# Kernel tuning notes

Hardware: AMD Instinct MI355X
Metric: run time of the kernel (lower is better)

## Reference

```python
import jax, jax.numpy as jnp
import numpy as np
from jax import lax

B, T, CIN, FN, H, W = 8, 8, 64, 64, 32, 32
GROUPS = 4 * FN // 32  # 8


def group_norm(x, g, b, groups, eps=1e-5):
    Bn, C, Hh, Ww = x.shape
    xr = x.reshape(Bn, groups, C // groups, Hh, Ww)
    mu = xr.mean(axis=(2, 3, 4), keepdims=True)
    var = xr.var(axis=(2, 3, 4), keepdims=True)
    xn = ((xr - mu) * lax.rsqrt(var + eps)).reshape(Bn, C, Hh, Ww)
    return xn * g[None, :, None, None] + b[None, :, None, None]


def conv1x1(x, w, b):
    # x: [B,C,H,W], w: [O,C]
    return jnp.einsum('bchw,oc->bohw', x, w) + b[None, :, None, None]


def setup_inputs() -> dict:
    key = jax.random.key(0)
    ks = jax.random.split(key, 8)
    s = 0.05
    return {
        'inputs': jax.random.normal(ks[0], (B, T, CIN, H, W), jnp.float32),
        'conv_w': jax.random.normal(ks[1], (4 * FN, CIN + FN, 3, 3), jnp.float32) * s,
        'conv_b': jnp.zeros((4 * FN,), jnp.float32),
        'gn_g': jnp.ones((4 * FN,), jnp.float32),
        'gn_b': jnp.zeros((4 * FN,), jnp.float32),
        'h_w': jax.random.normal(ks[2], (3 * FN, FN), jnp.float32) * s,
        'h_b': jnp.zeros((3 * FN,), jnp.float32),
        'm_w': jax.random.normal(ks[3], (2 * FN, FN), jnp.float32) * s,
        'm_b': jnp.zeros((2 * FN,), jnp.float32),
        'z1_w': jax.random.normal(ks[4], (FN, 2 * FN), jnp.float32) * s,
        'z1_b': jnp.zeros((FN,), jnp.float32),
        'z2_w': jax.random.normal(ks[5], (3 * FN, 2 * FN), jnp.float32) * s,
        'z2_b': jnp.zeros((3 * FN,), jnp.float32),
    }


def _sam(oh, im, h_w, h_b, m_w, m_b, z1_w, z1_b, z2_w, z2_b):
    Bn, C, Hh, Ww = oh.shape
    HW = Hh * Ww
    h_qkv = conv1x1(oh, h_w, h_b)  # [B,3C,H,W]
    m_kv = conv1x1(im, m_w, m_b)   # [B,2C,H,W]
    Qh, Kh, Vh = jnp.split(h_qkv, 3, axis=1)
    Km, Vm = jnp.split(m_kv, 2, axis=1)
    Q = Qh.reshape(Bn, C, HW).transpose(0, 2, 1)  # [B,HW,C]
    Kh = Kh.reshape(Bn, C, HW)
    Vh = Vh.reshape(Bn, C, HW)
    Km = Km.reshape(Bn, C, HW)
    Vm = Vm.reshape(Bn, C, HW)
    Ah = jax.nn.softmax(jnp.einsum('bnc,bcm->bnm', Q, Kh), axis=-1)  # [B,HW,HW]
    Am = jax.nn.softmax(jnp.einsum('bnc,bcm->bnm', Q, Km), axis=-1)
    Zh = jnp.einsum('bcn,bnm->bcm', Vh, Ah)  # [B,C,HW]
    Zm = jnp.einsum('bcn,bnm->bcm', Vm, Am)
    Zcat = jnp.concatenate([Zh, Zm], axis=1).reshape(Bn, 2 * C, Hh, Ww)
    Z = conv1x1(Zcat, z1_w, z1_b)  # [B,C,H,W]
    gates = conv1x1(jnp.concatenate([Z, oh], axis=1), z2_w, z2_b)  # [B,3C,H,W]
    o, g, i = jnp.split(gates, 3, axis=1)
    i = jax.nn.sigmoid(i)
    om = jnp.tanh(g) * i + (1.0 - i) * im
    oh2 = jax.nn.sigmoid(o) * om
    return oh2, om


def reference(inputs, conv_w, conv_b, gn_g, gn_b, h_w, h_b, m_w, m_b, z1_w, z1_b, z2_w, z2_b):
    Bn = inputs.shape[0]
    Hh, Ww = inputs.shape[-2], inputs.shape[-1]
    ih0 = jnp.zeros((Bn, FN, Hh, Ww), inputs.dtype)
    ic0 = jnp.zeros_like(ih0)
    im0 = jnp.zeros_like(ih0)

    def step(carry, x):
        ih, ic, im = carry
        comb = jnp.concatenate([x, ih], axis=1)
        gates = lax.conv_general_dilated(
            comb, conv_w, window_strides=(1, 1), padding='SAME',
            dimension_numbers=('NCHW', 'OIHW', 'NCHW')) + conv_b[None, :, None, None]
        gates = group_norm(gates, gn_g, gn_b, GROUPS)
        ingate, forgetgate, cellgate, outgate = jnp.split(gates, 4, axis=1)
        oc = ic * jax.nn.sigmoid(forgetgate) + jax.nn.sigmoid(ingate) * jnp.tanh(cellgate)
        oh = jax.nn.sigmoid(outgate) * jnp.tanh(oc)
        oh, om = _sam(oh, im, h_w, h_b, m_w, m_b, z1_w, z1_b, z2_w, z2_b)
        return (oh, oc, om), oh

    xs = jnp.moveaxis(inputs, 1, 0)  # [T,B,C,H,W]
    (ohT, ocT, imT), ys = lax.scan(step, (ih0, ic0, im0), xs)
    out = jnp.moveaxis(ys, 0, 1)  # [B,T,FN,H,W]
    return out, (ohT, ocT, imT)
```

## Files before the change

kernel.cpp:

```cpp
#include <hip/hip_runtime.h>
#include <math.h>


#define DEV __device__ __forceinline__

DEV float sigm(float x) { return 1.0f / (1.0f + __expf(-x)); }

DEV unsigned short f2bf(float f) {
  union { float f; unsigned u; } v; v.f = f;
  unsigned r = v.u + 0x7FFF + ((v.u >> 16) & 1);
  return (unsigned short)(r >> 16);
}

DEV unsigned pk2(float a, float b) {
  return (unsigned)f2bf(a) | ((unsigned)f2bf(b) << 16);
}

typedef float f32x4 __attribute__((ext_vector_type(4)));
typedef short bf16x8 __attribute__((ext_vector_type(8)));

#define FMA16(A, av, bv) do { \
  A[0][0] = fmaf(av.x, bv.x, A[0][0]); A[0][1] = fmaf(av.x, bv.y, A[0][1]); \
  A[0][2] = fmaf(av.x, bv.z, A[0][2]); A[0][3] = fmaf(av.x, bv.w, A[0][3]); \
  A[1][0] = fmaf(av.y, bv.x, A[1][0]); A[1][1] = fmaf(av.y, bv.y, A[1][1]); \
  A[1][2] = fmaf(av.y, bv.z, A[1][2]); A[1][3] = fmaf(av.y, bv.w, A[1][3]); \
  A[2][0] = fmaf(av.z, bv.x, A[2][0]); A[2][1] = fmaf(av.z, bv.y, A[2][1]); \
  A[2][2] = fmaf(av.z, bv.z, A[2][2]); A[2][3] = fmaf(av.z, bv.w, A[2][3]); \
  A[3][0] = fmaf(av.w, bv.x, A[3][0]); A[3][1] = fmaf(av.w, bv.y, A[3][1]); \
  A[3][2] = fmaf(av.w, bv.z, A[3][2]); A[3][3] = fmaf(av.w, bv.w, A[3][3]); \
} while (0)

__global__ __launch_bounds__(256) void wprep_kernel(
    const float* __restrict__ w, unsigned short* __restrict__ wpack)
{
  int e = blockIdx.x * 256 + threadIdx.x;
  int ci = e % 40;   int r = e / 40;
  int ocl = r % 128; r /= 128;
  int s = r % 36;    int oh = r / 36;
  int chh = s / 18;
  int t2  = s % 18;
  int tap = t2 >> 1, kc = t2 & 1;
  unsigned short v = 0;
  if (ci < 32) {
    int oc = oh * 128 + ocl;
    int c  = chh * 64 + kc * 32 + ci;
    v = f2bf(w[(size_t)(oc * 128 + c) * 9 + tap]);
  }
  wpack[e] = v;
}

__global__ __launch_bounds__(256) void conv3_mfma_kernel(
    const float* __restrict__ x,
    const float* __restrict__ ihb,
    const unsigned short* __restrict__ wpack,
    const float* __restrict__ bias,
    float* __restrict__ gates, int t)
{
  int ptile = blockIdx.x;
  int b     = blockIdx.y;
  int oh    = blockIdx.z;

  __shared__ __align__(16) unsigned short img[4 * 34 * 136];
  __shared__ __align__(16) unsigned short wbuf[2][128 * 40];

  int tid  = threadIdx.x;
  int lane = tid & 63;
  int wv   = tid >> 6;
  int mrow = wv >> 1, ncol = wv & 1;
  int y0 = ptile * 2;

  for (int i = tid; i < 4 * 34 * 136 / 2; i += 256) ((unsigned*)img)[i] = 0u;
  __syncthreads();

  const float* xsrc = x + (size_t)(b * 8 + t) * 65536;
  const float* hsrc = ihb + (size_t)b * 65536;
#pragma unroll
  for (int i = 0; i < 16; ++i) {
    int u = tid + i * 256;
    int ch = u >> 5;
    int v5 = u & 31;
    int row = v5 >> 3;
    int col4 = (v5 & 7) * 4;
    int gy = y0 - 1 + row;
    if (gy >= 0 && gy < 32) {
      const float* src = (ch < 64) ? (xsrc + (size_t)ch * 1024)
                                   : (hsrc + (size_t)(ch - 64) * 1024);
      float4 f = *(const float4*)(src + gy * 32 + col4);
      int base = (row * 34 + col4 + 1) * 136 + ch;
      img[base]       = f2bf(f.x);
      img[base + 136] = f2bf(f.y);
      img[base + 272] = f2bf(f.z);
      img[base + 408] = f2bf(f.w);
    }
  }

  const unsigned* wsl = (const unsigned*)wpack + (size_t)oh * 36 * 2560;
  unsigned* wb32 = (unsigned*)&wbuf[0][0];
#pragma unroll
  for (int k2 = 0; k2 < 10; ++k2)
    wb32[tid + k2 * 256] = wsl[tid + k2 * 256];
  __syncthreads();

  int aoff = (mrow * 64 + (lane & 15)) * 40 + (lane >> 4) * 8;
  int pb[2];
#pragma unroll
  for (int nf = 0; nf < 2; ++nf) {
    int pp = ncol * 32 + nf * 16 + (lane & 15);
    int rr = pp >> 5, cc = pp & 31;
    pb[nf] = (rr * 34 + cc) * 136 + (lane >> 4) * 8;
  }

  f32x4 acc[4][2] = {};
  unsigned wreg[10];

#pragma unroll
  for (int s = 0; s < 36; ++s) {
    int cur = s & 1;
    if (s < 35) {
      const unsigned* nsl = wsl + (s + 1) * 2560;
#pragma unroll
      for (int k2 = 0; k2 < 10; ++k2) wreg[k2] = nsl[tid + k2 * 256];
    }
    int chh = s / 18;
    int t2  = s % 18;
    int tap = t2 >> 1, kc = t2 & 1;
    int dy = tap / 3, dx = tap % 3;
    int toff = (dy * 34 + dx) * 136 + chh * 64 + kc * 32;

    bf16x8 a[4], bb[2];
#pragma unroll
    for (int mf = 0; mf < 4; ++mf)
      a[mf] = *(const bf16x8*)&wbuf[cur][aoff + mf * 640];
#pragma unroll
    for (int nf = 0; nf < 2; ++nf)
      bb[nf] = *(const bf16x8*)&img[pb[nf] + toff];
#pragma unroll
    for (int mf = 0; mf < 4; ++mf)
#pragma unroll
      for (int nf = 0; nf < 2; ++nf)
        acc[mf][nf] = __builtin_amdgcn_mfma_f32_16x16x32_bf16(
            a[mf], bb[nf], acc[mf][nf], 0, 0, 0);

    if (s < 35) {
      unsigned* dst = (unsigned*)&wbuf[0][0] + (1 - cur) * 2560;
#pragma unroll
      for (int k2 = 0; k2 < 10; ++k2) dst[tid + k2 * 256] = wreg[k2];
    }
    __syncthreads();
  }

  int orow_base = oh * 128 + mrow * 64 + (lane >> 4) * 4;
  int pcol = ptile * 64 + ncol * 32 + (lane & 15);
  float* gout = gates + (size_t)b * 262144;
#pragma unroll
  for (int mf = 0; mf < 4; ++mf)
#pragma unroll
    for (int nf = 0; nf < 2; ++nf)
#pragma unroll
      for (int r = 0; r < 4; ++r) {
        int oc_ = orow_base + mf * 16 + r;
        gout[(size_t)oc_ * 1024 + pcol + nf * 16] = acc[mf][nf][r] + bias[oc_];
      }
}

__global__ __launch_bounds__(256) void gnstats_kernel(
    const float* __restrict__ g, float* __restrict__ st)
{
  int grp = blockIdx.x; int b = blockIdx.y;
  const float* p0 = g + (size_t)b * 262144 + (size_t)grp * 32768;
  float s = 0.0f, q = 0.0f;
  for (int i = threadIdx.x; i < 8192; i += 256) {
    float4 a = *(const float4*)(p0 + (size_t)i * 4);
    s += a.x + a.y + a.z + a.w;
    q += a.x * a.x + a.y * a.y + a.z * a.z + a.w * a.w;
  }
#pragma unroll
  for (int off = 32; off > 0; off >>= 1) {
    s += __shfl_down(s, off);
    q += __shfl_down(q, off);
  }
  __shared__ float ss[4], qq[4];
  int wid = threadIdx.x >> 6;
  if ((threadIdx.x & 63) == 0) { ss[wid] = s; qq[wid] = q; }
  __syncthreads();
  if (threadIdx.x == 0) {
    float S = ss[0] + ss[1] + ss[2] + ss[3];
    float Q = qq[0] + qq[1] + qq[2] + qq[3];
    float mu = S / 32768.0f;
    float var = Q / 32768.0f - mu * mu;
    st[(b * 8 + grp) * 2]     = mu;
    st[(b * 8 + grp) * 2 + 1] = rsqrtf(var + 1e-5f);
  }
}

__global__ __launch_bounds__(256) void gnlstm_kernel(
    const float* __restrict__ g,
    const float* __restrict__ st, const float* __restrict__ gn_g,
    const float* __restrict__ gn_b, float* __restrict__ ic,
    float* __restrict__ cat2, float* __restrict__ out)
{
  int c = blockIdx.x; int b = blockIdx.y;
  int px = threadIdx.x * 4;
  size_t base = (size_t)b * 262144 + (size_t)c * 1024 + px;

  float4 vi4 = *(const float4*)(g + base);
  float4 vf4 = *(const float4*)(g + base + 65536);
  float4 vc4 = *(const float4*)(g + base + 131072);
  float4 vo4 = *(const float4*)(g + base + 196608);

  int ch0 = c, ch1 = 64 + c, ch2 = 128 + c, ch3 = 192 + c;
  float mu, is;
  mu = st[(b * 8 + (ch0 >> 5)) * 2]; is = st[(b * 8 + (ch0 >> 5)) * 2 + 1];
  float ga0 = gn_g[ch0] * is, bb0 = gn_b[ch0] - mu * ga0;
  mu = st[(b * 8 + (ch1 >> 5)) * 2]; is = st[(b * 8 + (ch1 >> 5)) * 2 + 1];
  float ga1 = gn_g[ch1] * is, bb1 = gn_b[ch1] - mu * ga1;
  mu = st[(b * 8 + (ch2 >> 5)) * 2]; is = st[(b * 8 + (ch2 >> 5)) * 2 + 1];
  float ga2 = gn_g[ch2] * is, bb2 = gn_b[ch2] - mu * ga2;
  mu = st[(b * 8 + (ch3 >> 5)) * 2]; is = st[(b * 8 + (ch3 >> 5)) * 2 + 1];
  float ga3 = gn_g[ch3] * is, bb3 = gn_b[ch3] - mu * ga3;

  size_t sb = (size_t)b * 65536 + (size_t)c * 1024 + px;
  float4 icv = *(const float4*)(ic + sb);
  float* vip = (float*)&vi4; float* vfp = (float*)&vf4;
  float* vcp = (float*)&vc4; float* vop = (float*)&vo4;
  float* icp = (float*)&icv;
  float4 ocv, ohv;
  float* ocp = (float*)&ocv; float* ohp = (float*)&ohv;
#pragma unroll
  for (int j = 0; j < 4; ++j) {
    float ing = sigm(vip[j] * ga0 + bb0);
    float fg  = sigm(vfp[j] * ga1 + bb1);
    float cg  = tanhf(vcp[j] * ga2 + bb2);
    float og  = sigm(vop[j] * ga3 + bb3);
    float oc  = icp[j] * fg + ing * cg;
    ocp[j] = oc;
    ohp[j] = og * tanhf(oc);
  }
  *(float4*)(ic + sb) = ocv;
  *(float4*)(out + 4718592 + sb) = ocv;
  *(float4*)(cat2 + (size_t)b * 131072 + (size_t)(64 + c) * 1024 + px) = ohv;
}

__global__ __launch_bounds__(256) void gemm_kernel(
    const float* __restrict__ W, const float* __restrict__ X,
    const float* __restrict__ bias,
    float* __restrict__ C, int K, int xbs, int cbs)
{
  int nt = blockIdx.x, mt = blockIdx.y, b = blockIdx.z;
  __shared__ float Xs[64 * 64];
  __shared__ float Wt[64 * 68];
  int tid = threadIdx.x;
  int mq = tid >> 4, nq = tid & 15;
  float acc[4][4] = {};
  const float* Xb  = X + (size_t)b * xbs + nt * 64;

  for (int k0 = 0; k0 < K; k0 += 64) {
    __syncthreads();
#pragma unroll
    for (int i = 0; i < 4; ++i) {
      int f = tid + i * 256;
      int kr = f >> 4; int nc = (f & 15) * 4;
      float4 v = *(const float4*)(Xb + (size_t)(k0 + kr) * 1024 + nc);
      *(float4*)&Xs[kr * 64 + nc] = v;
      int mr = kr; int kc = nc;
      float4 wv = *(const float4*)(W + (size_t)(mt * 64 + mr) * K + k0 + kc);
      Wt[(kc + 0) * 68 + mr] = wv.x;
      Wt[(kc + 1) * 68 + mr] = wv.y;
      Wt[(kc + 2) * 68 + mr] = wv.z;
      Wt[(kc + 3) * 68 + mr] = wv.w;
    }
    __syncthreads();
#pragma unroll 8
    for (int kk = 0; kk < 64; ++kk) {
      float4 wv = *(float4*)&Wt[kk * 68 + mq * 4];
      float4 xv = *(float4*)&Xs[kk * 64 + nq * 4];
      FMA16(acc, wv, xv);
    }
  }
  float* Cb = C + (size_t)b * cbs + (size_t)(mt * 64 + mq * 4) * 1024 + nt * 64 + nq * 4;
#pragma unroll
  for (int i = 0; i < 4; ++i) {
    float bv = bias ? bias[mt * 64 + mq * 4 + i] : 0.0f;
    float4 o = make_float4(acc[i][0] + bv, acc[i][1] + bv,
                           acc[i][2] + bv, acc[i][3] + bv);
    *(float4*)(Cb + (size_t)i * 1024) = o;
  }
}

__global__ __launch_bounds__(256) void att_stats_kernel(
    const float* __restrict__ qkv, const float* __restrict__ mkv,
    float* __restrict__ stats)
{
  int nt = blockIdx.x, att = blockIdx.y, b = blockIdx.z;
  const float* Qb = qkv + (size_t)b * 196608;
  const float* Kb = att ? (mkv + (size_t)b * 131072)
                        : (qkv + (size_t)b * 196608 + 65536);
  __shared__ __align__(16) unsigned short Qs[64 * 72];
  __shared__ __align__(16) unsigned short Ks[64 * 72];
  int tid = threadIdx.x, lane = tid & 63, w = tid >> 6;
  int n0 = nt * 64;

#pragma unroll
  for (int i = 0; i < 8; ++i) {
    int u = tid + i * 256;
    int c2 = u >> 6, nl = u & 63;
    float f0 = Qb[(size_t)(2 * c2) * 1024 + n0 + nl];
    float f1 = Qb[(size_t)(2 * c2 + 1) * 1024 + n0 + nl];
    ((unsigned*)Qs)[nl * 36 + c2] = pk2(f0, f1);
  }
  __syncthreads();
  bf16x8 qa0 = *(const bf16x8*)&Qs[(w * 16 + (lane & 15)) * 72 + (lane >> 4) * 8];
  bf16x8 qa1 = *(const bf16x8*)&Qs[(w * 16 + (lane & 15)) * 72 + 32 + (lane >> 4) * 8];

  float M[4] = {-3.0e38f, -3.0e38f, -3.0e38f, -3.0e38f};
  float Dsum[4] = {0.f, 0.f, 0.f, 0.f};

  for (int mt = 0; mt < 16; ++mt) {
    __syncthreads();
#pragma unroll
    for (int i = 0; i < 8; ++i) {
      int u = tid + i * 256;
      int c2 = u >> 6, ml = u & 63;
      float f0 = Kb[(size_t)(2 * c2) * 1024 + mt * 64 + ml];
      float f1 = Kb[(size_t)(2 * c2 + 1) * 1024 + mt * 64 + ml];
      ((unsigned*)Ks)[ml * 36 + c2] = pk2(f0, f1);
    }
    __syncthreads();
    f32x4 s[4];
#pragma unroll
    for (int mf = 0; mf < 4; ++mf) {
      bf16x8 b0 = *(const bf16x8*)&Ks[(mf * 16 + (lane & 15)) * 72 + (lane >> 4) * 8];
      bf16x8 b1 = *(const bf16x8*)&Ks[(mf * 16 + (lane & 15)) * 72 + 32 + (lane >> 4) * 8];
      f32x4 tacc = {};
      tacc = __builtin_amdgcn_mfma_f32_16x16x32_bf16(qa0, b0, tacc, 0, 0, 0);
      tacc = __builtin_amdgcn_mfma_f32_16x16x32_bf16(qa1, b1, tacc, 0, 0, 0);
      s[mf] = tacc;
    }
#pragma unroll
    for (int r = 0; r < 4; ++r) {
      float v0 = s[0][r], v1 = s[1][r], v2 = s[2][r], v3 = s[3][r];
      float mx = fmaxf(fmaxf(v0, v1), fmaxf(v2, v3));
      float nm = fmaxf(M[r], mx);
      Dsum[r] = Dsum[r] * __expf(M[r] - nm) +
                __expf(v0 - nm) + __expf(v1 - nm) +
                __expf(v2 - nm) + __expf(v3 - nm);
      M[r] = nm;
    }
  }
#pragma unroll
  for (int off = 1; off < 16; off <<= 1) {
#pragma unroll
    for (int r = 0; r < 4; ++r) {
      float Mo = __shfl_xor(M[r], off);
      float Do = __shfl_xor(Dsum[r], off);
      float nm = fmaxf(M[r], Mo);
      Dsum[r] = Dsum[r] * __expf(M[r] - nm) + Do * __expf(Mo - nm);
      M[r] = nm;
    }
  }
  if ((lane & 15) == 0) {
    float* stb = stats + (size_t)(b * 2 + att) * 2048;
#pragma unroll
    for (int r = 0; r < 4; ++r) {
      int n = n0 + w * 16 + (lane >> 4) * 4 + r;
      stb[n] = M[r];
      stb[1024 + n] = 1.0f / Dsum[r];
    }
  }
}

__global__ __launch_bounds__(256) void att_z_kernel(
    const float* __restrict__ qkv, const float* __restrict__ mkv,
    const float* __restrict__ stats, float* __restrict__ zc)
{
  int mt = blockIdx.x, att = blockIdx.y, b = blockIdx.z;
  const float* Qb = qkv + (size_t)b * 196608;
  const float* Kb = att ? (mkv + (size_t)b * 131072)
                        : (qkv + (size_t)b * 196608 + 65536);
  const float* Vb = att ? (mkv + (size_t)b * 131072 + 65536)
                        : (qkv + (size_t)b * 196608 + 131072);
  const float* stM = stats + (size_t)(b * 2 + att) * 2048;
  const float* stR = stM + 1024;

  __shared__ __align__(16) unsigned short Ks[64 * 72];
  __shared__ __align__(16) unsigned short Qs[64 * 72];
  __shared__ __align__(16) unsigned short Vs[64 * 72];
  __shared__ __align__(16) unsigned short Ps[64 * 72];
  __shared__ float Mn[64];

  int tid = threadIdx.x, lane = tid & 63, w = tid >> 6;
  int m0 = mt * 64;

#pragma unroll
  for (int i = 0; i < 8; ++i) {
    int u = tid + i * 256;
    int c2 = u >> 6, ml = u & 63;
    float f0 = Kb[(size_t)(2 * c2) * 1024 + m0 + ml];
    float f1 = Kb[(size_t)(2 * c2 + 1) * 1024 + m0 + ml];
    ((unsigned*)Ks)[ml * 36 + c2] = pk2(f0, f1);
  }
  __syncthreads();
  bf16x8 bk[4][2];
#pragma unroll
  for (int mf = 0; mf < 4; ++mf) {
    bk[mf][0] = *(const bf16x8*)&Ks[(mf * 16 + (lane & 15)) * 72 + (lane >> 4) * 8];
    bk[mf][1] = *(const bf16x8*)&Ks[(mf * 16 + (lane & 15)) * 72 + 32 + (lane >> 4) * 8];
  }

  f32x4 zacc[4] = {};

  for (int ntb = 0; ntb < 16; ++ntb) {
    int n0 = ntb * 64;
    __syncthreads();
#pragma unroll
    for (int i = 0; i < 8; ++i) {
      int u = tid + i * 256;
      int c2 = u >> 6, nl = u & 63;
      float f0 = Qb[(size_t)(2 * c2) * 1024 + n0 + nl];
      float f1 = Qb[(size_t)(2 * c2 + 1) * 1024 + n0 + nl];
      ((unsigned*)Qs)[nl * 36 + c2] = pk2(f0, f1);
    }
#pragma unroll
    for (int i = 0; i < 4; ++i) {
      int u = tid + i * 256;
      int c = u >> 4, n4 = (u & 15) * 4;
      float4 v = *(const float4*)(Vb + (size_t)c * 1024 + n0 + n4);
      float4 rv = *(const float4*)(stR + n0 + n4);
      unsigned* dst = (unsigned*)&Vs[c * 72 + n4];
      dst[0] = pk2(v.x * rv.x, v.y * rv.y);
      dst[1] = pk2(v.z * rv.z, v.w * rv.w);
    }
    if (tid < 64) Mn[tid] = stM[n0 + tid];
    __syncthreads();

    bf16x8 qa0 = *(const bf16x8*)&Qs[(w * 16 + (lane & 15)) * 72 + (lane >> 4) * 8];
    bf16x8 qa1 = *(const bf16x8*)&Qs[(w * 16 + (lane & 15)) * 72 + 32 + (lane >> 4) * 8];
    float mr[4];
#pragma unroll
    for (int r = 0; r < 4; ++r) mr[r] = Mn[w * 16 + (lane >> 4) * 4 + r];
#pragma unroll
    for (int mf = 0; mf < 4; ++mf) {
      f32x4 tacc = {};
      tacc = __builtin_amdgcn_mfma_f32_16x16x32_bf16(qa0, bk[mf][0], tacc, 0, 0, 0);
      tacc = __builtin_amdgcn_mfma_f32_16x16x32_bf16(qa1, bk[mf][1], tacc, 0, 0, 0);
      unsigned* dst = (unsigned*)&Ps[(mf * 16 + (lane & 15)) * 72 +
                                     w * 16 + (lane >> 4) * 4];
      dst[0] = pk2(__expf(tacc[0] - mr[0]), __expf(tacc[1] - mr[1]));
      dst[1] = pk2(__expf(tacc[2] - mr[2]), __expf(tacc[3] - mr[3]));
    }
    __syncthreads();

    bf16x8 va0 = *(const bf16x8*)&Vs[(w * 16 + (lane & 15)) * 72 + (lane >> 4) * 8];
    bf16x8 va1 = *(const bf16x8*)&Vs[(w * 16 + (lane & 15)) * 72 + 32 + (lane >> 4) * 8];
#pragma unroll
    for (int mf = 0; mf < 4; ++mf) {
      bf16x8 p0 = *(const bf16x8*)&Ps[(mf * 16 + (lane & 15)) * 72 + (lane >> 4) * 8];
      bf16x8 p1 = *(const bf16x8*)&Ps[(mf * 16 + (lane & 15)) * 72 + 32 + (lane >> 4) * 8];
      zacc[mf] = __builtin_amdgcn_mfma_f32_16x16x32_bf16(va0, p0, zacc[mf], 0, 0, 0);
      zacc[mf] = __builtin_amdgcn_mfma_f32_16x16x32_bf16(va1, p1, zacc[mf], 0, 0, 0);
    }
  }

  float* zb = zc + (size_t)b * 131072 + (size_t)att * 65536;
#pragma unroll
  for (int mf = 0; mf < 4; ++mf)
#pragma unroll
    for (int r = 0; r < 4; ++r) {
      int c = w * 16 + (lane >> 4) * 4 + r;
      zb[(size_t)c * 1024 + m0 + mf * 16 + (lane & 15)] = zacc[mf][r];
    }
}

__global__ __launch_bounds__(256) void sam_kernel(
    const float* __restrict__ g2, float* __restrict__ im,
    float* __restrict__ ih, float* __restrict__ out, int t)
{
  int c = blockIdx.x; int b = blockIdx.y;
  int px = threadIdx.x * 4;
  size_t gb = (size_t)b * 196608 + (size_t)c * 1024 + px;
  float4 vo4 = *(const float4*)(g2 + gb);
  float4 vg4 = *(const float4*)(g2 + gb + 65536);
  float4 vi4 = *(const float4*)(g2 + gb + 131072);
  size_t sb = (size_t)b * 65536 + (size_t)c * 1024 + px;
  float4 vm4 = *(const float4*)(im + sb);
  float* vop = (float*)&vo4; float* vgp = (float*)&vg4;
  float* vip = (float*)&vi4; float* vmp = (float*)&vm4;
  float4 om4, oh4;
  float* omp = (float*)&om4; float* ohp = (float*)&oh4;
#pragma unroll
  for (int j = 0; j < 4; ++j) {
    float ig = sigm(vip[j]);
    float om = tanhf(vgp[j]) * ig + (1.0f - ig) * vmp[j];
    omp[j] = om;
    ohp[j] = sigm(vop[j]) * om;
  }
  *(float4*)(im + sb) = om4;
  *(float4*)(ih + sb) = oh4;
  *(float4*)(out + ((size_t)(b * 8 + t) * 64 + c) * 1024 + px) = oh4;
  *(float4*)(out + 4194304 + sb) = oh4;
  *(float4*)(out + 5242880 + sb) = om4;
}

extern "C" void kernel_launch(void* const* d_in, const int* in_sizes, int n_in,
                              void* d_out, int out_size, void* d_ws,
                              size_t ws_size, hipStream_t stream)
{
  const float* x      = (const float*)d_in[0];
  const float* conv_w = (const float*)d_in[1];
  const float* conv_b = (const float*)d_in[2];
  const float* gn_g   = (const float*)d_in[3];
  const float* gn_b   = (const float*)d_in[4];
  const float* h_w    = (const float*)d_in[5];
  const float* h_b    = (const float*)d_in[6];
  const float* m_w    = (const float*)d_in[7];
  const float* m_b    = (const float*)d_in[8];
  const float* z1_w   = (const float*)d_in[9];
  const float* z1_b   = (const float*)d_in[10];
  const float* z2_w   = (const float*)d_in[11];
  const float* z2_b   = (const float*)d_in[12];
  float* out = (float*)d_out;
  float* ws  = (float*)d_ws;

  float* ic     = ws;
  float* ih     = ws + 524288;
  float* im     = ws + 1048576;
  float* gates  = ws + 1572864;
  float* gnst   = ws + 3670016;
  float* qkv    = ws + 3670272;
  float* mkv    = ws + 5243136;
  float* stats  = ws + 6291712;
  float* cat2   = ws + 6357248;
  float* zc     = ws + 7405824;
  unsigned short* wpack = (unsigned short*)(ws + 8454400);
  float* g2     = gates;

  hipMemsetAsync(ic, 0, (size_t)3 * 524288 * sizeof(float), stream);
  wprep_kernel<<<dim3(1440), 256, 0, stream>>>(conv_w, wpack);

  for (int t = 0; t < 8; ++t) {
    conv3_mfma_kernel<<<dim3(16, 8, 2), 256, 0, stream>>>(
        x, ih, wpack, conv_b, gates, t);
    gnstats_kernel<<<dim3(8, 8), 256, 0, stream>>>(gates, gnst);
    gnlstm_kernel<<<dim3(64, 8), 256, 0, stream>>>(gates, gnst, gn_g,
                                                   gn_b, ic, cat2, out);
    gemm_kernel<<<dim3(16, 3, 8), 256, 0, stream>>>(
        h_w, cat2 + 65536, h_b, qkv, 64, 131072, 196608);
    gemm_kernel<<<dim3(16, 2, 8), 256, 0, stream>>>(
        m_w, im, m_b, mkv, 64, 65536, 131072);
    att_stats_kernel<<<dim3(16, 2, 8), 256, 0, stream>>>(qkv, mkv, stats);
    att_z_kernel<<<dim3(16, 2, 8), 256, 0, stream>>>(qkv, mkv, stats, zc);
    gemm_kernel<<<dim3(16, 1, 8), 256, 0, stream>>>(
        z1_w, zc, z1_b, cat2, 128, 131072, 131072);
    gemm_kernel<<<dim3(16, 3, 8), 256, 0, stream>>>(
        z2_w, cat2, z2_b, g2, 128, 131072, 196608);
    sam_kernel<<<dim3(64, 8), 256, 0, stream>>>(g2, im, ih, out, t);
  }
}
```

Before: 1.132 ms.

## Use bf16 MFMA for 1x1 projections and split attention over key halves

The scalar-FMA 1x1 projection GEMMs are replaced by a bf16 MFMA kernel. The projection weights are pre-packed to bf16 once per call. The attention stats and Z kernels now split the key/query range into two halves, doubling the grid from 256 to 512 blocks. Partial softmax statistics are merged inside att_z, and the two partial Z outputs are summed while loading in the z1 GEMM. This aims to raise occupancy on a small grid and cut the FP32 GEMM cost, at the price of extra bf16 rounding in the projections and extra workspace traffic.

```diff
diff --git a/kernel.cpp b/kernel.cpp
--- a/kernel.cpp
+++ b/kernel.cpp
@@ -18,17 +18,6 @@
 
 typedef float f32x4 __attribute__((ext_vector_type(4)));
 typedef short bf16x8 __attribute__((ext_vector_type(8)));
-
-#define FMA16(A, av, bv) do { \
-  A[0][0] = fmaf(av.x, bv.x, A[0][0]); A[0][1] = fmaf(av.x, bv.y, A[0][1]); \
-  A[0][2] = fmaf(av.x, bv.z, A[0][2]); A[0][3] = fmaf(av.x, bv.w, A[0][3]); \
-  A[1][0] = fmaf(av.y, bv.x, A[1][0]); A[1][1] = fmaf(av.y, bv.y, A[1][1]); \
-  A[1][2] = fmaf(av.y, bv.z, A[1][2]); A[1][3] = fmaf(av.y, bv.w, A[1][3]); \
-  A[2][0] = fmaf(av.z, bv.x, A[2][0]); A[2][1] = fmaf(av.z, bv.y, A[2][1]); \
-  A[2][2] = fmaf(av.z, bv.z, A[2][2]); A[2][3] = fmaf(av.z, bv.w, A[2][3]); \
-  A[3][0] = fmaf(av.w, bv.x, A[3][0]); A[3][1] = fmaf(av.w, bv.y, A[3][1]); \
-  A[3][2] = fmaf(av.w, bv.z, A[3][2]); A[3][3] = fmaf(av.w, bv.w, A[3][3]); \
-} while (0)
 
 __global__ __launch_bounds__(256) void wprep_kernel(
     const float* __restrict__ w, unsigned short* __restrict__ wpack)
@@ -47,6 +36,21 @@
     v = f2bf(w[(size_t)(oc * 128 + c) * 9 + tap]);
   }
   wpack[e] = v;
+}
+
+__global__ __launch_bounds__(256) void wproj_kernel(
+    const float* __restrict__ h_w, const float* __restrict__ m_w,
+    const float* __restrict__ z1_w, const float* __restrict__ z2_w,
+    unsigned short* __restrict__ wp)
+{
+  int e = blockIdx.x * 256 + threadIdx.x;
+  if (e >= 53248) return;
+  float v;
+  if (e < 12288)       v = h_w[e];
+  else if (e < 20480)  v = m_w[e - 12288];
+  else if (e < 28672)  v = z1_w[e - 20480];
+  else                 v = z2_w[e - 28672];
+  wp[e] = f2bf(v);
 }
 
 __global__ __launch_bounds__(256) void conv3_mfma_kernel(
@@ -241,57 +245,66 @@
   *(float4*)(cat2 + (size_t)b * 131072 + (size_t)(64 + c) * 1024 + px) = ohv;
 }
 
-__global__ __launch_bounds__(256) void gemm_kernel(
-    const float* __restrict__ W, const float* __restrict__ X,
-    const float* __restrict__ bias,
+__global__ __launch_bounds__(256) void gemm_mfma_kernel(
+    const unsigned short* __restrict__ Wp, const float* __restrict__ X,
+    const float* __restrict__ X2, const float* __restrict__ bias,
     float* __restrict__ C, int K, int xbs, int cbs)
 {
   int nt = blockIdx.x, mt = blockIdx.y, b = blockIdx.z;
-  __shared__ float Xs[64 * 64];
-  __shared__ float Wt[64 * 68];
-  int tid = threadIdx.x;
-  int mq = tid >> 4, nq = tid & 15;
-  float acc[4][4] = {};
-  const float* Xb  = X + (size_t)b * xbs + nt * 64;
-
-  for (int k0 = 0; k0 < K; k0 += 64) {
-    __syncthreads();
-#pragma unroll
-    for (int i = 0; i < 4; ++i) {
-      int f = tid + i * 256;
-      int kr = f >> 4; int nc = (f & 15) * 4;
-      float4 v = *(const float4*)(Xb + (size_t)(k0 + kr) * 1024 + nc);
-      *(float4*)&Xs[kr * 64 + nc] = v;
-      int mr = kr; int kc = nc;
-      float4 wv = *(const float4*)(W + (size_t)(mt * 64 + mr) * K + k0 + kc);
-      Wt[(kc + 0) * 68 + mr] = wv.x;
-      Wt[(kc + 1) * 68 + mr] = wv.y;
-      Wt[(kc + 2) * 68 + mr] = wv.z;
-      Wt[(kc + 3) * 68 + mr] = wv.w;
-    }
-    __syncthreads();
-#pragma unroll 8
-    for (int kk = 0; kk < 64; ++kk) {
-      float4 wv = *(float4*)&Wt[kk * 68 + mq * 4];
-      float4 xv = *(float4*)&Xs[kk * 64 + nq * 4];
-      FMA16(acc, wv, xv);
-    }
-  }
-  float* Cb = C + (size_t)b * cbs + (size_t)(mt * 64 + mq * 4) * 1024 + nt * 64 + nq * 4;
-#pragma unroll
-  for (int i = 0; i < 4; ++i) {
-    float bv = bias ? bias[mt * 64 + mq * 4 + i] : 0.0f;
-    float4 o = make_float4(acc[i][0] + bv, acc[i][1] + bv,
-                           acc[i][2] + bv, acc[i][3] + bv);
-    *(float4*)(Cb + (size_t)i * 1024) = o;
-  }
+  __shared__ __align__(16) unsigned short Xs[64 * 136];
+  int tid = threadIdx.x, lane = tid & 63, w = tid >> 6;
+  int n0 = nt * 64;
+  int kstride = K + 8;
+  const float* Xb  = X + (size_t)b * xbs;
+  const float* X2b = X2 ? (X2 + (size_t)b * xbs) : nullptr;
+
+  int niter = K / 8;
+  for (int i = 0; i < niter; ++i) {
+    int u = tid + i * 256;
+    int c2 = u >> 6, nl = u & 63;
+    float f0 = Xb[(size_t)(2 * c2) * 1024 + n0 + nl];
+    float f1 = Xb[(size_t)(2 * c2 + 1) * 1024 + n0 + nl];
+    if (X2b) {
+      f0 += X2b[(size_t)(2 * c2) * 1024 + n0 + nl];
+      f1 += X2b[(size_t)(2 * c2 + 1) * 1024 + n0 + nl];
+    }
+    ((unsigned*)Xs)[nl * (kstride / 2) + c2] = pk2(f0, f1);
+  }
+  __syncthreads();
+
+  int mrow = mt * 64 + w * 16 + (lane & 15);
+  bf16x8 ka[4];
+  int nks = K / 32;
+  for (int ks = 0; ks < nks; ++ks)
+    ka[ks] = *(const bf16x8*)&Wp[(size_t)mrow * K + ks * 32 + (lane >> 4) * 8];
+
+  f32x4 acc[4] = {};
+#pragma unroll
+  for (int nf = 0; nf < 4; ++nf) {
+    for (int ks = 0; ks < nks; ++ks) {
+      bf16x8 bx = *(const bf16x8*)&Xs[(nf * 16 + (lane & 15)) * kstride +
+                                      ks * 32 + (lane >> 4) * 8];
+      acc[nf] = __builtin_amdgcn_mfma_f32_16x16x32_bf16(ka[ks], bx, acc[nf], 0, 0, 0);
+    }
+  }
+
+  float* Cb = C + (size_t)b * cbs;
+#pragma unroll
+  for (int nf = 0; nf < 4; ++nf)
+#pragma unroll
+    for (int r = 0; r < 4; ++r) {
+      int m = mt * 64 + w * 16 + (lane >> 4) * 4 + r;
+      Cb[(size_t)m * 1024 + n0 + nf * 16 + (lane & 15)] = acc[nf][r] + bias[m];
+    }
 }
 
 __global__ __launch_bounds__(256) void att_stats_kernel(
     const float* __restrict__ qkv, const float* __restrict__ mkv,
     float* __restrict__ stats)
 {
-  int nt = blockIdx.x, att = blockIdx.y, b = blockIdx.z;
+  int nt = blockIdx.x;
+  int att = blockIdx.y >> 1, mh = blockIdx.y & 1;
+  int b = blockIdx.z;
   const float* Qb = qkv + (size_t)b * 196608;
   const float* Kb = att ? (mkv + (size_t)b * 131072)
                         : (qkv + (size_t)b * 196608 + 65536);
@@ -315,7 +328,7 @@
   float M[4] = {-3.0e38f, -3.0e38f, -3.0e38f, -3.0e38f};
   float Dsum[4] = {0.f, 0.f, 0.f, 0.f};
 
-  for (int mt = 0; mt < 16; ++mt) {
+  for (int mt = mh * 8; mt < mh * 8 + 8; ++mt) {
     __syncthreads();
 #pragma unroll
     for (int i = 0; i < 8; ++i) {
@@ -359,34 +372,37 @@
     }
   }
   if ((lane & 15) == 0) {
-    float* stb = stats + (size_t)(b * 2 + att) * 2048;
+    float* stb = stats + (size_t)(((b * 2 + att) * 2 + mh) * 2) * 1024;
 #pragma unroll
     for (int r = 0; r < 4; ++r) {
       int n = n0 + w * 16 + (lane >> 4) * 4 + r;
       stb[n] = M[r];
-      stb[1024 + n] = 1.0f / Dsum[r];
+      stb[1024 + n] = Dsum[r];
     }
   }
 }
 
 __global__ __launch_bounds__(256) void att_z_kernel(
     const float* __restrict__ qkv, const float* __restrict__ mkv,
-    const float* __restrict__ stats, float* __restrict__ zc)
-{
-  int mt = blockIdx.x, att = blockIdx.y, b = blockIdx.z;
+    const float* __restrict__ stats, float* __restrict__ zc0,
+    float* __restrict__ zc1)
+{
+  int mt = blockIdx.x;
+  int att = blockIdx.y >> 1, nh = blockIdx.y & 1;
+  int b = blockIdx.z;
   const float* Qb = qkv + (size_t)b * 196608;
   const float* Kb = att ? (mkv + (size_t)b * 131072)
                         : (qkv + (size_t)b * 196608 + 65536);
   const float* Vb = att ? (mkv + (size_t)b * 131072 + 65536)
                         : (qkv + (size_t)b * 196608 + 131072);
-  const float* stM = stats + (size_t)(b * 2 + att) * 2048;
-  const float* stR = stM + 1024;
+  const float* stb = stats + (size_t)(b * 2 + att) * 4096;
 
   __shared__ __align__(16) unsigned short Ks[64 * 72];
   __shared__ __align__(16) unsigned short Qs[64 * 72];
   __shared__ __align__(16) unsigned short Vs[64 * 72];
   __shared__ __align__(16) unsigned short Ps[64 * 72];
   __shared__ float Mn[64];
+  __shared__ float Rn[64];
 
   int tid = threadIdx.x, lane = tid & 63, w = tid >> 6;
   int m0 = mt * 64;
@@ -409,9 +425,18 @@
 
   f32x4 zacc[4] = {};
 
-  for (int ntb = 0; ntb < 16; ++ntb) {
+  for (int ntb = nh * 8; ntb < nh * 8 + 8; ++ntb) {
     int n0 = ntb * 64;
     __syncthreads();
+    if (tid < 64) {
+      int n = n0 + tid;
+      float M0 = stb[n],        D0 = stb[1024 + n];
+      float M1 = stb[2048 + n], D1 = stb[3072 + n];
+      float Mm = fmaxf(M0, M1);
+      float Dm = D0 * __expf(M0 - Mm) + D1 * __expf(M1 - Mm);
+      Mn[tid] = Mm;
+      Rn[tid] = 1.0f / Dm;
+    }
 #pragma unroll
     for (int i = 0; i < 8; ++i) {
       int u = tid + i * 256;
@@ -420,18 +445,16 @@
       float f1 = Qb[(size_t)(2 * c2 + 1) * 1024 + n0 + nl];
       ((unsigned*)Qs)[nl * 36 + c2] = pk2(f0, f1);
     }
+    __syncthreads();
 #pragma unroll
     for (int i = 0; i < 4; ++i) {
       int u = tid + i * 256;
       int c = u >> 4, n4 = (u & 15) * 4;
       float4 v = *(const float4*)(Vb + (size_t)c * 1024 + n0 + n4);
-      float4 rv = *(const float4*)(stR + n0 + n4);
       unsigned* dst = (unsigned*)&Vs[c * 72 + n4];
-      dst[0] = pk2(v.x * rv.x, v.y * rv.y);
-      dst[1] = pk2(v.z * rv.z, v.w * rv.w);
-    }
-    if (tid < 64) Mn[tid] = stM[n0 + tid];
-    __syncthreads();
+      dst[0] = pk2(v.x * Rn[n4], v.y * Rn[n4 + 1]);
+      dst[1] = pk2(v.z * Rn[n4 + 2], v.w * Rn[n4 + 3]);
+    }
 
     bf16x8 qa0 = *(const bf16x8*)&Qs[(w * 16 + (lane & 15)) * 72 + (lane >> 4) * 8];
     bf16x8 qa1 = *(const bf16x8*)&Qs[(w * 16 + (lane & 15)) * 72 + 32 + (lane >> 4) * 8];
@@ -461,7 +484,7 @@
     }
   }
 
-  float* zb = zc + (size_t)b * 131072 + (size_t)att * 65536;
+  float* zb = (nh ? zc1 : zc0) + (size_t)b * 131072 + (size_t)att * 65536;
 #pragma unroll
   for (int mf = 0; mf < 4; ++mf)
 #pragma unroll
@@ -530,12 +553,20 @@
   float* mkv    = ws + 5243136;
   float* stats  = ws + 6291712;
   float* cat2   = ws + 6357248;
-  float* zc     = ws + 7405824;
+  float* zc0    = ws + 7405824;
   unsigned short* wpack = (unsigned short*)(ws + 8454400);
+  unsigned short* wproj = (unsigned short*)(ws + 8638720);
+  float* zc1    = ws + 8665344;
   float* g2     = gates;
+
+  const unsigned short* hp  = wproj;
+  const unsigned short* mp  = wproj + 12288;
+  const unsigned short* z1p = wproj + 20480;
+  const unsigned short* z2p = wproj + 28672;
 
   hipMemsetAsync(ic, 0, (size_t)3 * 524288 * sizeof(float), stream);
   wprep_kernel<<<dim3(1440), 256, 0, stream>>>(conv_w, wpack);
+  wproj_kernel<<<dim3(208), 256, 0, stream>>>(h_w, m_w, z1_w, z2_w, wproj);
 
   for (int t = 0; t < 8; ++t) {
     conv3_mfma_kernel<<<dim3(16, 8, 2), 256, 0, stream>>>(
@@ -543,16 +574,16 @@
     gnstats_kernel<<<dim3(8, 8), 256, 0, stream>>>(gates, gnst);
     gnlstm_kernel<<<dim3(64, 8), 256, 0, stream>>>(gates, gnst, gn_g,
                                                    gn_b, ic, cat2, out);
-    gemm_kernel<<<dim3(16, 3, 8), 256, 0, stream>>>(
-        h_w, cat2 + 65536, h_b, qkv, 64, 131072, 196608);
-    gemm_kernel<<<dim3(16, 2, 8), 256, 0, stream>>>(
-        m_w, im, m_b, mkv, 64, 65536, 131072);
-    att_stats_kernel<<<dim3(16, 2, 8), 256, 0, stream>>>(qkv, mkv, stats);
-    att_z_kernel<<<dim3(16, 2, 8), 256, 0, stream>>>(qkv, mkv, stats, zc);
-    gemm_kernel<<<dim3(16, 1, 8), 256, 0, stream>>>(
-        z1_w, zc, z1_b, cat2, 128, 131072, 131072);
-    gemm_kernel<<<dim3(16, 3, 8), 256, 0, stream>>>(
-        z2_w, cat2, z2_b, g2, 128, 131072, 196608);
+    gemm_mfma_kernel<<<dim3(16, 3, 8), 256, 0, stream>>>(
+        hp, cat2 + 65536, nullptr, h_b, qkv, 64, 131072, 196608);
+    gemm_mfma_kernel<<<dim3(16, 2, 8), 256, 0, stream>>>(
+        mp, im, nullptr, m_b, mkv, 64, 65536, 131072);
+    att_stats_kernel<<<dim3(16, 4, 8), 256, 0, stream>>>(qkv, mkv, stats);
+    att_z_kernel<<<dim3(16, 4, 8), 256, 0, stream>>>(qkv, mkv, stats, zc0, zc1);
+    gemm_mfma_kernel<<<dim3(16, 1, 8), 256, 0, stream>>>(
+        z1p, zc0, zc1, z1_b, cat2, 128, 131072, 131072);
+    gemm_mfma_kernel<<<dim3(16, 3, 8), 256, 0, stream>>>(
+        z2p, cat2, nullptr, z2_b, g2, 128, 131072, 196608);
     sam_kernel<<<dim3(64, 8), 256, 0, stream>>>(g2, im, ih, out, t);
   }
 }
```

New measurement: 2.393 ms. 2.11x slower.
